# Kernel tuning notes

Hardware: AMD Instinct MI355X
Metric: run time of the kernel (lower is better)

The kernel has to match this reference:

```python
import jax, jax.numpy as jnp
import numpy as np

OUT_SIZE = 7
SPATIAL_SCALE = 0.0625
SAMPLE_NUM = 2


def setup_inputs() -> dict:
    key = jax.random.key(0)
    k1, k2, k3, k4, k5, k6 = jax.random.split(key, 6)
    N, C, H, W = 4, 256, 96, 96
    K = 1024
    features = jax.random.normal(k1, (N, C, H, W), dtype=jnp.float32)
    img_h, img_w = H / SPATIAL_SCALE, W / SPATIAL_SCALE
    batch_idx = jax.random.randint(k2, (K,), 0, N).astype(jnp.float32)
    x1 = jax.random.uniform(k3, (K,)) * (img_w - 320.0)
    y1 = jax.random.uniform(k4, (K,)) * (img_h - 320.0)
    x2 = x1 + 16.0 + jax.random.uniform(k5, (K,)) * 300.0
    y2 = y1 + 16.0 + jax.random.uniform(k6, (K,)) * 300.0
    rois = jnp.stack([batch_idx, x1, y1, x2, y2], axis=1).astype(jnp.float32)
    return {"features": features, "rois": rois}


def _sample_coords(start, bin_size):
    # start, bin_size: [K]; returns [K, OUT_SIZE*SAMPLE_NUM] sample-point coords
    g = jnp.arange(OUT_SIZE * SAMPLE_NUM, dtype=jnp.float32)
    bin_idx = jnp.floor(g / SAMPLE_NUM)
    sub = g - bin_idx * SAMPLE_NUM
    offs = bin_idx + (sub + 0.5) / SAMPLE_NUM
    return start[:, None] + bin_size[:, None] * offs[None, :]


def _interp_1d(coord, size):
    # coord: [K, G] sample coords along one axis of a map of length `size`.
    valid = (coord >= -1.0) & (coord <= jnp.float32(size))
    c = jnp.clip(coord, 0.0, jnp.float32(size - 1))
    lo = jnp.floor(c)
    hi = jnp.minimum(lo + 1.0, jnp.float32(size - 1))
    frac = c - lo  # weight of hi; (1-frac) weight of lo
    return lo.astype(jnp.int32), hi.astype(jnp.int32), frac, valid


def roi_align(features, rois):
    N, C, H, W = features.shape
    b = rois[:, 0].astype(jnp.int32)
    x1, y1, x2, y2 = (rois[:, i] * SPATIAL_SCALE for i in (1, 2, 3, 4))
    roi_w = jnp.maximum(x2 - x1, 1.0)
    roi_h = jnp.maximum(y2 - y1, 1.0)
    bin_w = roi_w / OUT_SIZE
    bin_h = roi_h / OUT_SIZE

    ys = _sample_coords(y1, bin_h)  # [K, G]
    xs = _sample_coords(x1, bin_w)  # [K, G]
    ylo, yhi, fy, vy = _interp_1d(ys, H)
    xlo, xhi, fx, vx = _interp_1d(xs, W)

    bb = b[:, None, None]

    def gather(yi, xi):
        # -> [K, G, G, C]
        return features[bb, :, yi[:, :, None], xi[:, None, :]]

    wy_lo, wy_hi = (1.0 - fy), fy
    wx_lo, wx_hi = (1.0 - fx), fx

    def w2(wy, wx):
        return (wy[:, :, None] * wx[:, None, :])[..., None]

    val = (gather(ylo, xlo) * w2(wy_lo, wx_lo)
           + gather(ylo, xhi) * w2(wy_lo, wx_hi)
           + gather(yhi, xlo) * w2(wy_hi, wx_lo)
           + gather(yhi, xhi) * w2(wy_hi, wx_hi))
    mask = (vy[:, :, None] & vx[:, None, :])[..., None]
    val = jnp.where(mask, val, 0.0)

    K = rois.shape[0]
    G = OUT_SIZE * SAMPLE_NUM
    val = val.reshape(K, OUT_SIZE, SAMPLE_NUM, OUT_SIZE, SAMPLE_NUM, C)
    out = val.mean(axis=(2, 4))          # average the sample points per bin
    return jnp.transpose(out, (0, 3, 1, 2))  # [K, C, out, out]


def reference(features, rois):
    return roi_align(features, rois)
```

## Files before the change

kernel.cpp:

```cpp
#include <hip/hip_runtime.h>

#define CCH   256
#define FH    96
#define FW    96
#define HW    (FH*FW)
#define SCALE 0.0625f

#define HROWS 21
#define SQMAX 7
#define PLANE (HROWS*SQMAX*4)
#define WCH   32

__global__ void bucket_rois(const float* __restrict__ rois, int* __restrict__ perm, int K)
{
    __shared__ int cnt[4], base[4];
    const int t = threadIdx.x;
    if (t < 4) cnt[t] = 0;
    __syncthreads();
    int b = 0, pos = 0;
    if (t < K) {
        b   = min(max((int)rois[t*5], 0), 3);
        pos = atomicAdd(&cnt[b], 1);
    }
    __syncthreads();
    if (t == 0) {
        int s = 0;
        #pragma unroll
        for (int i = 0; i < 4; ++i) { base[i] = s; s += cnt[i]; }
    }
    __syncthreads();
    if (t < K) perm[base[b] + pos] = t;
}

__global__ __launch_bounds__(256, 8)
void roialign_kernel(const float* __restrict__ feat,
                     const float* __restrict__ rois,
                     float* __restrict__ out,
                     const int* __restrict__ perm)
{
    __shared__ __align__(16) float win[4 * PLANE];
    __shared__ int   s_lo[2][14];
    __shared__ float s_wl[2][14], s_wh[2][14];

    const int xcd  = blockIdx.x & 7;
    const int j    = blockIdx.x >> 3;
    const int q    = ((xcd >> 1) << 8) + j;
    const int half = xcd & 1;
    const int k    = perm ? perm[q] : q;

    const int tid  = threadIdx.x;
    const int w    = tid >> 6;
    const int ll   = tid & 63;

    const float x1 = rois[k*5+1] * SCALE;
    const float y1 = rois[k*5+2] * SCALE;
    const float x2 = rois[k*5+3] * SCALE;
    const float y2 = rois[k*5+4] * SCALE;
    const int   b  = (int)rois[k*5+0];
    const float binw = fmaxf(x2 - x1, 1.0f) * (1.0f/7.0f);
    const float binh = fmaxf(y2 - y1, 1.0f) * (1.0f/7.0f);

    if (tid < 28) {
        const int   axis  = (tid >= 14) ? 1 : 0;
        const int   g     = axis ? tid - 14 : tid;
        const float start = axis ? x1 : y1;
        const float bsz   = axis ? binw : binh;
        const float offs  = (float)(g >> 1) + 0.25f + 0.5f*(float)(g & 1);
        const float coord = start + bsz * offs;
        const bool  valid = (coord >= -1.0f) && (coord <= 96.0f);
        const float cc    = fminf(fmaxf(coord, 0.0f), 95.0f);
        const float lof   = floorf(cc);
        const float frac  = cc - lof;
        const float v     = valid ? 1.0f : 0.0f;
        s_lo[axis][g] = (int)lof;
        s_wl[axis][g] = (1.0f - frac) * v;
        s_wh[axis][g] = frac * v;
    }
    __syncthreads();

    const int row0   = s_lo[0][0];
    const int col0   = s_lo[1][0] & ~3;
    const int colEnd = min(s_lo[1][13] + 1, FW-1);
    const int width  = colEnd - col0 + 1;
    const int cwq    = min((width + 3) >> 2, 6);
    const int sQ     = ((cwq + 1) & ~1) | 1;
    const int RS     = sQ * 4;
    int hw_          = min(s_lo[0][13] + 1, FH-1) - row0 + 1;
    const int hwin   = min(hw_, HROWS);
    const int nslot  = hwin * cwq;

    float* const wp = &win[w * PLANE];

    {
        const float4 z = make_float4(0.f, 0.f, 0.f, 0.f);
        #pragma unroll
        for (int jj = 0; jj < 3; ++jj) {
            const int qq = ll + 64*jj;
            if (qq < PLANE/4) *(float4*)&wp[qq*4] = z;
        }
    }

    const bool active = ll < 49;
    const int  p  = active ? ll : 0;
    const int  oy = p / 7;
    const int  ox = p - oy*7;

    int   aL[4], aH[4];
    float w00[4], w01[4], w10[4], w11[4];
    #pragma unroll
    for (int sy = 0; sy < 2; ++sy) {
        const int   gy  = 2*oy + sy;
        const int   rlo = min(s_lo[0][gy] - row0,                 HROWS-1);
        const int   rhi = min(min(s_lo[0][gy]+1, FH-1) - row0,    HROWS-1);
        const float wyl = s_wl[0][gy], wyh = s_wh[0][gy];
        #pragma unroll
        for (int sx = 0; sx < 2; ++sx) {
            const int   gx  = 2*ox + sx;
            const int   clo = min(s_lo[1][gx] - col0, RS-2);
            const float wxl = s_wl[1][gx], wxh = s_wh[1][gx];
            const int   s   = sy*2 + sx;
            aL[s] = rlo*RS + clo;
            aH[s] = rhi*RS + clo;
            w00[s] = wyl*wxl*0.25f;  w01[s] = wyl*wxh*0.25f;
            w10[s] = wyh*wxl*0.25f;  w11[s] = wyh*wxh*0.25f;
        }
    }

    const int  sl1 = ll + 64;
    const int  r0  = ll  / cwq, q0 = ll  - r0*cwq;
    const int  r1  = sl1 / cwq, q1 = sl1 - r1*cwq;
    const bool L0  = ll  < nslot;
    const bool L1  = sl1 < nslot;
    const int  goff0 = min(row0 + r0, FH-1)*FW + col0 + q0*4;
    const int  goff1 = min(row0 + r1, FH-1)*FW + col0 + q1*4;
    const int  ld0   = min(r0, HROWS-1)*RS + q0*4;
    const int  ld1   = min(r1, HROWS-1)*RS + q1*4;

    const int    cb   = half*128 + w*WCH;
    const float* gch  = feat + (size_t)(b*CCH + cb) * HW;
    float*       outp = out  + ((size_t)k*CCH + cb)*49 + p;

    float4 st0, st1;
    if (L0) st0 = *(const float4*)(gch + goff0);
    if (L1) st1 = *(const float4*)(gch + goff1);

    for (int c = 0; c < WCH; ++c) {
        if (L0) *(float4*)&wp[ld0] = st0;
        if (L1) *(float4*)&wp[ld1] = st1;

        if (c + 1 < WCH) {
            const float* gn = gch + (size_t)(c+1)*HW;
            if (L0) st0 = *(const float4*)(gn + goff0);
            if (L1) st1 = *(const float4*)(gn + goff1);
        }

        if (active) {
            float t0 = w00[0]*wp[aL[0]]   + w01[0]*wp[aL[0]+1]
                     + w10[0]*wp[aH[0]]   + w11[0]*wp[aH[0]+1];
            float t1 = w00[1]*wp[aL[1]]   + w01[1]*wp[aL[1]+1]
                     + w10[1]*wp[aH[1]]   + w11[1]*wp[aH[1]+1];
            float t2 = w00[2]*wp[aL[2]]   + w01[2]*wp[aL[2]+1]
                     + w10[2]*wp[aH[2]]   + w11[2]*wp[aH[2]+1];
            float t3 = w00[3]*wp[aL[3]]   + w01[3]*wp[aL[3]+1]
                     + w10[3]*wp[aH[3]]   + w11[3]*wp[aH[3]+1];
            outp[0] = (t0 + t1) + (t2 + t3);
        }
        outp += 49;
    }
}

extern "C" void kernel_launch(void* const* d_in, const int* in_sizes, int n_in,
                              void* d_out, int out_size, void* d_ws, size_t ws_size,
                              hipStream_t stream) {
    const float* feat = (const float*)d_in[0];
    const float* rois = (const float*)d_in[1];
    float*       outp = (float*)d_out;
    const int K = in_sizes[1] / 5;

    int* perm = nullptr;
    if (d_ws && ws_size >= (size_t)K * sizeof(int) && K <= 1024) {
        perm = (int*)d_ws;
        bucket_rois<<<1, 1024, 0, stream>>>(rois, perm, K);
    }
    roialign_kernel<<<K*2, 256, 0, stream>>>(feat, rois, outp, perm);
}
```

Before: 132.0 us.

## Separate bilinear interpolation into row pass in registers and column pass in LDS

Splits the 2D bilinear sampling into two passes. The vertical interpolation (four row loads per slot, weighted by y weights with the 1/4 averaging folded in) is done in registers before writing to LDS. The LDS window then shrinks from up to 21 raw rows to 7 pre-reduced rows, and each output only does horizontal interpolation from LDS. This cuts LDS footprint, zero-fill and per-output reads, and drops the old 21-row clamp on tall ROIs. In exchange each loader thread issues four global loads per channel instead of up to two, and rows can be fetched more than once.

```diff
diff --git a/kernel.cpp b/kernel.cpp
--- a/kernel.cpp
+++ b/kernel.cpp
@@ -6,9 +6,8 @@
 #define HW    (FH*FW)
 #define SCALE 0.0625f
 
-#define HROWS 21
 #define SQMAX 7
-#define PLANE (HROWS*SQMAX*4)
+#define PLANE (7*SQMAX*4)
 #define WCH   32
 
 __global__ void bucket_rois(const float* __restrict__ rois, int* __restrict__ perm, int K)
@@ -71,99 +70,88 @@
         const float cc    = fminf(fmaxf(coord, 0.0f), 95.0f);
         const float lof   = floorf(cc);
         const float frac  = cc - lof;
-        const float v     = valid ? 1.0f : 0.0f;
+        const float v     = valid ? (axis ? 1.0f : 0.25f) : 0.0f;
         s_lo[axis][g] = (int)lof;
         s_wl[axis][g] = (1.0f - frac) * v;
         s_wh[axis][g] = frac * v;
     }
     __syncthreads();
 
-    const int row0   = s_lo[0][0];
     const int col0   = s_lo[1][0] & ~3;
     const int colEnd = min(s_lo[1][13] + 1, FW-1);
     const int width  = colEnd - col0 + 1;
     const int cwq    = min((width + 3) >> 2, 6);
     const int sQ     = ((cwq + 1) & ~1) | 1;
     const int RS     = sQ * 4;
-    int hw_          = min(s_lo[0][13] + 1, FH-1) - row0 + 1;
-    const int hwin   = min(hw_, HROWS);
-    const int nslot  = hwin * cwq;
+    const int nslot  = 7 * cwq;
 
     float* const wp = &win[w * PLANE];
 
-    {
-        const float4 z = make_float4(0.f, 0.f, 0.f, 0.f);
-        #pragma unroll
-        for (int jj = 0; jj < 3; ++jj) {
-            const int qq = ll + 64*jj;
-            if (qq < PLANE/4) *(float4*)&wp[qq*4] = z;
-        }
-    }
+    if (ll < PLANE/4) *(float4*)&wp[ll*4] = make_float4(0.f, 0.f, 0.f, 0.f);
 
     const bool active = ll < 49;
     const int  p  = active ? ll : 0;
     const int  oy = p / 7;
     const int  ox = p - oy*7;
-
-    int   aL[4], aH[4];
-    float w00[4], w01[4], w10[4], w11[4];
-    #pragma unroll
-    for (int sy = 0; sy < 2; ++sy) {
-        const int   gy  = 2*oy + sy;
-        const int   rlo = min(s_lo[0][gy] - row0,                 HROWS-1);
-        const int   rhi = min(min(s_lo[0][gy]+1, FH-1) - row0,    HROWS-1);
-        const float wyl = s_wl[0][gy], wyh = s_wh[0][gy];
-        #pragma unroll
-        for (int sx = 0; sx < 2; ++sx) {
-            const int   gx  = 2*ox + sx;
-            const int   clo = min(s_lo[1][gx] - col0, RS-2);
-            const float wxl = s_wl[1][gx], wxh = s_wh[1][gx];
-            const int   s   = sy*2 + sx;
-            aL[s] = rlo*RS + clo;
-            aH[s] = rhi*RS + clo;
-            w00[s] = wyl*wxl*0.25f;  w01[s] = wyl*wxh*0.25f;
-            w10[s] = wyh*wxl*0.25f;  w11[s] = wyh*wxh*0.25f;
-        }
+    float cw0, cw1, cw2, cw3;
+    int   ca0, ca1;
+    {
+        const int gx0 = 2*ox, gx1 = 2*ox + 1;
+        const int c0  = min(s_lo[1][gx0] - col0, RS-2);
+        const int c1  = min(s_lo[1][gx1] - col0, RS-2);
+        cw0 = s_wl[1][gx0];  cw1 = s_wh[1][gx0];
+        cw2 = s_wl[1][gx1];  cw3 = s_wh[1][gx1];
+        ca0 = oy*RS + c0;
+        ca1 = oy*RS + c1;
     }
 
-    const int  sl1 = ll + 64;
-    const int  r0  = ll  / cwq, q0 = ll  - r0*cwq;
-    const int  r1  = sl1 / cwq, q1 = sl1 - r1*cwq;
-    const bool L0  = ll  < nslot;
-    const bool L1  = sl1 < nslot;
-    const int  goff0 = min(row0 + r0, FH-1)*FW + col0 + q0*4;
-    const int  goff1 = min(row0 + r1, FH-1)*FW + col0 + q1*4;
-    const int  ld0   = min(r0, HROWS-1)*RS + q0*4;
-    const int  ld1   = min(r1, HROWS-1)*RS + q1*4;
+    const int  s   = min(ll, nslot - 1);
+    const int  soy = s / cwq;
+    const int  sq  = s - soy*cwq;
+    const bool st  = ll < nslot;
+    float sw0, sw1, sw2, sw3;
+    int   g0, g1, g2, g3;
+    {
+        const int gy0 = 2*soy, gy1 = 2*soy + 1;
+        const int rl0 = s_lo[0][gy0], rh0 = min(rl0 + 1, FH-1);
+        const int rl1 = s_lo[0][gy1], rh1 = min(rl1 + 1, FH-1);
+        sw0 = s_wl[0][gy0];  sw1 = s_wh[0][gy0];
+        sw2 = s_wl[0][gy1];  sw3 = s_wh[0][gy1];
+        const int cq = col0 + 4*sq;
+        g0 = rl0*FW + cq;  g1 = rh0*FW + cq;
+        g2 = rl1*FW + cq;  g3 = rh1*FW + cq;
+    }
+    const int ld = soy*RS + 4*sq;
 
     const int    cb   = half*128 + w*WCH;
     const float* gch  = feat + (size_t)(b*CCH + cb) * HW;
     float*       outp = out  + ((size_t)k*CCH + cb)*49 + p;
 
-    float4 st0, st1;
-    if (L0) st0 = *(const float4*)(gch + goff0);
-    if (L1) st1 = *(const float4*)(gch + goff1);
+    float4 A0, A1, A2, A3;
+    if (st) {
+        A0 = *(const float4*)(gch + g0);  A1 = *(const float4*)(gch + g1);
+        A2 = *(const float4*)(gch + g2);  A3 = *(const float4*)(gch + g3);
+    }
 
     for (int c = 0; c < WCH; ++c) {
-        if (L0) *(float4*)&wp[ld0] = st0;
-        if (L1) *(float4*)&wp[ld1] = st1;
+        if (st) {
+            float4 v;
+            v.x = sw0*A0.x + sw1*A1.x + sw2*A2.x + sw3*A3.x;
+            v.y = sw0*A0.y + sw1*A1.y + sw2*A2.y + sw3*A3.y;
+            v.z = sw0*A0.z + sw1*A1.z + sw2*A2.z + sw3*A3.z;
+            v.w = sw0*A0.w + sw1*A1.w + sw2*A2.w + sw3*A3.w;
+            *(float4*)&wp[ld] = v;
 
-        if (c + 1 < WCH) {
-            const float* gn = gch + (size_t)(c+1)*HW;
-            if (L0) st0 = *(const float4*)(gn + goff0);
-            if (L1) st1 = *(const float4*)(gn + goff1);
+            if (c + 1 < WCH) {
+                const float* gn = gch + (size_t)(c+1)*HW;
+                A0 = *(const float4*)(gn + g0);  A1 = *(const float4*)(gn + g1);
+                A2 = *(const float4*)(gn + g2);  A3 = *(const float4*)(gn + g3);
+            }
         }
 
         if (active) {
-            float t0 = w00[0]*wp[aL[0]]   + w01[0]*wp[aL[0]+1]
-                     + w10[0]*wp[aH[0]]   + w11[0]*wp[aH[0]+1];
-            float t1 = w00[1]*wp[aL[1]]   + w01[1]*wp[aL[1]+1]
-                     + w10[1]*wp[aH[1]]   + w11[1]*wp[aH[1]+1];
-            float t2 = w00[2]*wp[aL[2]]   + w01[2]*wp[aL[2]+1]
-                     + w10[2]*wp[aH[2]]   + w11[2]*wp[aH[2]+1];
-            float t3 = w00[3]*wp[aL[3]]   + w01[3]*wp[aL[3]+1]
-                     + w10[3]*wp[aH[3]]   + w11[3]*wp[aH[3]+1];
-            outp[0] = (t0 + t1) + (t2 + t3);
+            outp[0] = cw0*wp[ca0] + cw1*wp[ca0+1]
+                    + cw2*wp[ca1] + cw3*wp[ca1+1];
         }
         outp += 49;
     }
```

Measured after the change: 141.6 us. +7.2%, slower.
